# Performance work log

Hardware: AMD Instinct MI355X
Metric: run time of the kernel (lower is better)

Reference implementation:

```python
import jax, jax.numpy as jnp
import numpy as np

N, E, F, H = 50000, 800000, 128, 128

def silu(v):
    return v * jax.nn.sigmoid(v)

def setup_inputs() -> dict:
    key = jax.random.key(0)
    ks = jax.random.split(key, 16)
    def lin(k, fan_in, fan_out):
        s = 1.0 / np.sqrt(fan_in)
        kw, kb = jax.random.split(k)
        W = jax.random.uniform(kw, (fan_in, fan_out), jnp.float32, -s, s)
        b = jax.random.uniform(kb, (fan_out,), jnp.float32, -s, s)
        return W, b
    x = jax.random.normal(ks[0], (N, F), jnp.float32)
    pos = jax.random.normal(ks[1], (N, 3), jnp.float32)
    edge_index = jax.random.randint(ks[2], (2, E), 0, N, jnp.int64)
    We1, be1 = lin(ks[3], 2 * F + 1, H)
    We2, be2 = lin(ks[4], H, H)
    Wn1, bn1 = lin(ks[5], F + H, H)
    Wn2, bn2 = lin(ks[6], H, F)
    Wc, bc = lin(ks[7], H, 1)
    return {"x": x, "pos": pos, "We1": We1, "be1": be1, "We2": We2, "be2": be2,
            "Wn1": Wn1, "bn1": bn1, "Wn2": Wn2, "bn2": bn2, "Wc": Wc, "bc": bc,
            "edge_index": edge_index}

def reference(x, pos, We1, be1, We2, be2, Wn1, bn1, Wn2, bn2, Wc, bc, edge_index):
    row, col = edge_index[0], edge_index[1]
    rij = pos[row] - pos[col]                      # [E,3]
    dij = jnp.sum(rij ** 2, axis=-1, keepdims=True)  # [E,1]
    edge_input = jnp.concatenate([x[row], x[col], dij], axis=-1)  # [E,2F+1]
    m_ij = silu(silu(edge_input @ We1 + be1) @ We2 + be2)          # [E,H]
    agg = jax.ops.segment_sum(m_ij, row, num_segments=N)          # [N,H]
    x_new = silu(jnp.concatenate([x, agg], axis=-1) @ Wn1 + bn1) @ Wn2 + bn2  # [N,F]
    w_ij = silu(m_ij @ Wc + bc)                    # [E,1]
    trans = rij * w_ij                             # [E,3]
    delta = jax.ops.segment_sum(trans, row, num_segments=N)       # [N,3]
    pos_new = pos + 0.01 * delta
    return (x_new, pos_new)
```

## Files before the change

### kernel.cpp

```cpp
#include <hip/hip_runtime.h>
#include <hip/hip_bf16.h>
#include <stdint.h>
#include <string.h>

#define NN 50000
#define NE 800000
#define SCAN_B 200
#define SCAN_CH 250

typedef short bf8_t __attribute__((ext_vector_type(8)));
typedef float f32x4 __attribute__((ext_vector_type(4)));

__device__ __forceinline__ float silu_f(float v) {
    return v * __builtin_amdgcn_rcpf(1.0f + __expf(-v));
}

__device__ __forceinline__ unsigned int pack2bf(float a, float b) {
    __hip_bfloat162 h = __float22bfloat162_rn(make_float2(a, b));
    unsigned int u; memcpy(&u, &h, 4);
    return u;
}

__device__ __forceinline__ float bf_lo(unsigned int u) { return __uint_as_float(u << 16); }
__device__ __forceinline__ float bf_hi(unsigned int u) { return __uint_as_float(u & 0xffff0000u); }

union U4B { uint4 u; bf8_t b; };
__device__ __forceinline__ bf8_t as_bf8(uint4 u) { U4B x; x.u = u; return x.b; }

__global__ __launch_bounds__(64) void prep_w(const float* __restrict__ We1,
                                             const float* __restrict__ We2,
                                             const float* __restrict__ Wn1,
                                             const float* __restrict__ Wn2,
                                             unsigned short* __restrict__ wf1,
                                             unsigned short* __restrict__ wf2,
                                             unsigned short* __restrict__ wfn1,
                                             unsigned short* __restrict__ wfn2) {
    int b = blockIdx.x, lane = threadIdx.x;
    int q = lane >> 4, c = lane & 15;
    const float* W; unsigned short* dst; int f;
    if (b < 64)       { W = We1; f = b;       dst = wf1  + (size_t)f * 512; }
    else if (b < 96)  { W = We2; f = b - 64;  dst = wf2  + (size_t)f * 512; }
    else if (b < 160) { W = Wn1; f = b - 96;  dst = wfn1 + (size_t)f * 512; }
    else              { W = Wn2; f = b - 160; dst = wfn2 + (size_t)f * 512; }
    int s = f >> 3, mf = f & 7;
    int k0 = s * 32 + q * 8, col = mf * 16 + c;
    float v[8];
    #pragma unroll
    for (int i = 0; i < 8; ++i) v[i] = W[(size_t)(k0 + i) * 128 + col];
    uint4 o;
    o.x = pack2bf(v[0], v[1]); o.y = pack2bf(v[2], v[3]);
    o.z = pack2bf(v[4], v[5]); o.w = pack2bf(v[6], v[7]);
    *(uint4*)(dst + lane * 8) = o;
}

__global__ __launch_bounds__(256, 4) void prep_node(
    const float* __restrict__ x, const int* __restrict__ ei,
    const unsigned short* __restrict__ wf1, const float* __restrict__ be1,
    unsigned short* __restrict__ xbf, unsigned short* __restrict__ zbf,
    unsigned short* __restrict__ ybf, int* __restrict__ cnt)
{
    const int tid = threadIdx.x;
    const int n0 = blockIdx.x * 64;
    const char* w1 = (const char*)wf1;

    {
        int e0 = (blockIdx.x * 256 + tid) * 4;
        if (e0 < NE) {
            int4 r4 = *(const int4*)(ei + e0);
            atomicAdd(&cnt[r4.x], 1); atomicAdd(&cnt[r4.y], 1);
            atomicAdd(&cnt[r4.z], 1); atomicAdd(&cnt[r4.w], 1);
        }
    }

    {
        int node = n0 + (tid >> 2);
        if (node < NN) {
            const float* src = x + (size_t)node * 128 + (tid & 3) * 32;
            unsigned short* dst = xbf + (size_t)node * 128 + (tid & 3) * 32;
            #pragma unroll
            for (int j = 0; j < 4; ++j) {
                float4 v0 = *(const float4*)(src + j * 8);
                float4 v1 = *(const float4*)(src + j * 8 + 4);
                uint4 o;
                o.x = pack2bf(v0.x, v0.y); o.y = pack2bf(v0.z, v0.w);
                o.z = pack2bf(v1.x, v1.y); o.w = pack2bf(v1.z, v1.w);
                *(uint4*)(dst + j * 8) = o;
            }
        }
    }

    const int P = tid >> 6, lane = tid & 63;
    const int q = lane >> 4, e16 = lane & 15;
    const int oc_q = P * 32 + q * 4;

    int nloc[4]; unsigned nb[4];
    #pragma unroll
    for (int t = 0; t < 4; ++t) {
        int nl = t * 16 + e16; nloc[t] = nl;
        int node = n0 + nl; if (node >= NN) node = NN - 1;
        nb[t] = (unsigned)node;
    }

    f32x4 accz[2][4], accy[2][4];
    #pragma unroll
    for (int M = 0; M < 2; ++M) {
        float4 bi = *(const float4*)(be1 + oc_q + M * 16);
        #pragma unroll
        for (int t = 0; t < 4; ++t) {
            accz[M][t][0] = bi.x; accz[M][t][1] = bi.y; accz[M][t][2] = bi.z; accz[M][t][3] = bi.w;
            accy[M][t][0] = 0.f;  accy[M][t][1] = 0.f;  accy[M][t][2] = 0.f;  accy[M][t][3] = 0.f;
        }
    }

    #pragma unroll
    for (int s = 0; s < 4; ++s) {
        bf8_t bfr[4];
        #pragma unroll
        for (int t = 0; t < 4; ++t) {
            const float* src = x + ((size_t)nb[t]) * 128 + s * 32 + q * 8;
            float4 v0 = *(const float4*)src;
            float4 v1 = *(const float4*)(src + 4);
            uint4 o;
            o.x = pack2bf(v0.x, v0.y); o.y = pack2bf(v0.z, v0.w);
            o.z = pack2bf(v1.x, v1.y); o.w = pack2bf(v1.z, v1.w);
            bfr[t] = as_bf8(o);
        }
        #pragma unroll
        for (int M = 0; M < 2; ++M) {
            unsigned wz = ((unsigned)(s * 8 + P * 2 + M) << 10) + ((unsigned)lane << 4);
            unsigned wy = ((unsigned)((s + 4) * 8 + P * 2 + M) << 10) + ((unsigned)lane << 4);
            bf8_t afz = as_bf8(*(const uint4*)(w1 + wz));
            bf8_t afy = as_bf8(*(const uint4*)(w1 + wy));
            #pragma unroll
            for (int t = 0; t < 4; ++t) {
                accz[M][t] = __builtin_amdgcn_mfma_f32_16x16x32_bf16(afz, bfr[t], accz[M][t], 0, 0, 0);
                accy[M][t] = __builtin_amdgcn_mfma_f32_16x16x32_bf16(afy, bfr[t], accy[M][t], 0, 0, 0);
            }
        }
    }

    #pragma unroll
    for (int M = 0; M < 2; ++M) {
        #pragma unroll
        for (int t = 0; t < 4; ++t) {
            int node = n0 + nloc[t];
            if (node < NN) {
                uint2 pz, py;
                pz.x = pack2bf(accz[M][t][0], accz[M][t][1]);
                pz.y = pack2bf(accz[M][t][2], accz[M][t][3]);
                py.x = pack2bf(accy[M][t][0], accy[M][t][1]);
                py.y = pack2bf(accy[M][t][2], accy[M][t][3]);
                *(uint2*)(zbf + ((size_t)node << 7) + oc_q + M * 16) = pz;
                *(uint2*)(ybf + ((size_t)node << 7) + oc_q + M * 16) = py;
            }
        }
    }
}

__global__ __launch_bounds__(256) void scan_bsum(const int* __restrict__ cnt,
                                                 int* __restrict__ bsum) {
    __shared__ int red[4];
    int b = blockIdx.x, tid = threadIdx.x;
    int n = b * SCAN_CH + tid;
    int v = (tid < SCAN_CH) ? cnt[n] : 0;
    #pragma unroll
    for (int o = 32; o; o >>= 1) v += __shfl_down(v, o);
    if ((tid & 63) == 0) red[tid >> 6] = v;
    __syncthreads();
    if (tid == 0) bsum[b] = red[0] + red[1] + red[2] + red[3];
}

__global__ __launch_bounds__(256) void scan_write(const int* __restrict__ cnt,
                                                  const int* __restrict__ bsum,
                                                  int* __restrict__ off,
                                                  int* __restrict__ cur) {
    __shared__ int part[256];
    __shared__ int basered[4];
    int b = blockIdx.x, tid = threadIdx.x;
    int bv = (tid < b) ? bsum[tid] : 0;
    #pragma unroll
    for (int o = 32; o; o >>= 1) bv += __shfl_down(bv, o);
    if ((tid & 63) == 0) basered[tid >> 6] = bv;
    __syncthreads();
    int base = basered[0] + basered[1] + basered[2] + basered[3];
    int n = b * SCAN_CH + tid;
    int c = (tid < SCAN_CH) ? cnt[n] : 0;
    part[tid] = c;
    __syncthreads();
    #pragma unroll
    for (int d = 1; d < 256; d <<= 1) {
        int v = (tid >= d) ? part[tid - d] : 0;
        __syncthreads();
        part[tid] += v;
        __syncthreads();
    }
    if (tid < SCAN_CH) {
        int excl = base + part[tid] - c;
        off[n] = excl; cur[n] = excl;
    }
    if (b == SCAN_B - 1 && tid == SCAN_CH) off[NN] = NE;
}

__global__ __launch_bounds__(256) void egnn_scatter(const int* __restrict__ ei,
                                                    int* __restrict__ cur,
                                                    int2* __restrict__ rc_slot) {
    int e = blockIdx.x * 256 + threadIdx.x;
    if (e < NE) {
        int r = ei[e];
        int p = atomicAdd(&cur[r], 1);
        rc_slot[p] = make_int2(r, ei[NE + e]);
    }
}

__global__ __launch_bounds__(256, 4) void egnn_edge_mfma(
    const unsigned short* __restrict__ zbf, const unsigned short* __restrict__ ybf,
    const float* __restrict__ pos,
    const unsigned short* __restrict__ wf2,
    const float* __restrict__ We1,
    const float* __restrict__ be2, const float* __restrict__ Wc,
    const float* __restrict__ bc,
    const int2* __restrict__ rc_slot,
    float* __restrict__ agg, float* __restrict__ delta)
{
    __shared__ __align__(16) unsigned short HsBuf[9216];
    unsigned short* Hs = HsBuf;
    unsigned short* mT = HsBuf;
    __shared__ int   rows_s[64];
    __shared__ float rij_s[64][3];
    __shared__ float dij_s[64];
    __shared__ float wdot[64];
    __shared__ int   seg_node[64], seg_start[65];
    __shared__ unsigned long long smask;
    __shared__ int firstPartial, lastPartial;

    const int tid = threadIdx.x;
    const int e0 = blockIdx.x * 64;
    const char* zb = (const char*)zbf;
    const char* yb = (const char*)ybf;
    const char* w2 = (const char*)wf2;

    if (tid < 64) {
        int2 rc = rc_slot[e0 + tid];
        int r = rc.x;
        rows_s[tid] = r;
        float d = 0.f;
        #pragma unroll
        for (int k = 0; k < 3; ++k) {
            float rv = pos[r * 3 + k] - pos[rc.y * 3 + k];
            rij_s[tid][k] = rv; d += rv * rv;
        }
        dij_s[tid] = d;
        wdot[tid] = 0.f;
        seg_start[tid] = 64;
        if (tid == 0) seg_start[64] = 64;
        int prev = __shfl_up(r, 1);
        bool flag = (tid == 0) || (r != prev);
        unsigned long long b = __ballot(flag);
        int seg = __popcll(b & ((2ull << tid) - 1)) - 1;
        if (flag) { seg_node[seg] = r; seg_start[seg] = tid; }
        int r63 = __shfl(r, 63);
        if (tid == 0) {
            smask = b;
            firstPartial = (e0 > 0) && (rc_slot[e0 - 1].x == r);
            lastPartial  = (e0 + 64 < NE) && (rc_slot[e0 + 64].x == r63);
        }
    }

    const int P = tid >> 6, lane = tid & 63;
    const int q = lane >> 4, e16 = lane & 15;
    const int oc_q = P * 32 + q * 4;

    int eloc[4]; unsigned rb[4], cb[4];
    #pragma unroll
    for (int t = 0; t < 4; ++t) {
        int el = t * 16 + e16; eloc[t] = el;
        int2 rc = rc_slot[e0 + el];
        rb[t] = (unsigned)rc.x << 8;
        cb[t] = (unsigned)rc.y << 8;
    }

    uint2 uzr[2][4], uyr[2][4];
    #pragma unroll
    for (int M = 0; M < 2; ++M) {
        const unsigned cbyte = (unsigned)((oc_q + M * 16) << 1);
        #pragma unroll
        for (int t = 0; t < 4; ++t) {
            uzr[M][t] = *(const uint2*)(zb + rb[t] + cbyte);
            uyr[M][t] = *(const uint2*)(yb + cb[t] + cbyte);
        }
    }
    __syncthreads();

    #pragma unroll
    for (int M = 0; M < 2; ++M) {
        float4 w256 = *(const float4*)(We1 + (size_t)256 * 128 + oc_q + M * 16);
        #pragma unroll
        for (int t = 0; t < 4; ++t) {
            uint2 uz = uzr[M][t], uy = uyr[M][t];
            float d = dij_s[eloc[t]];
            float v0 = silu_f(bf_lo(uz.x) + bf_lo(uy.x) + d * w256.x);
            float v1 = silu_f(bf_hi(uz.x) + bf_hi(uy.x) + d * w256.y);
            float v2 = silu_f(bf_lo(uz.y) + bf_lo(uy.y) + d * w256.z);
            float v3 = silu_f(bf_hi(uz.y) + bf_hi(uy.y) + d * w256.w);
            uint2 pk; pk.x = pack2bf(v0, v1); pk.y = pack2bf(v2, v3);
            *(uint2*)(Hs + eloc[t] * 136 + oc_q + M * 16) = pk;
        }
    }
    __syncthreads();

    f32x4 acc2[2][4];
    #pragma unroll
    for (int M = 0; M < 2; ++M) {
        float4 bi = *(const float4*)(be2 + oc_q + M * 16);
        #pragma unroll
        for (int t = 0; t < 4; ++t) { acc2[M][t][0] = bi.x; acc2[M][t][1] = bi.y; acc2[M][t][2] = bi.z; acc2[M][t][3] = bi.w; }
    }

    #pragma unroll
    for (int s = 0; s < 4; ++s) {
        bf8_t bfr[4];
        #pragma unroll
        for (int t = 0; t < 4; ++t)
            bfr[t] = as_bf8(*(const uint4*)(Hs + eloc[t] * 136 + s * 32 + q * 8));
        __builtin_amdgcn_s_setprio(1);
        #pragma unroll
        for (int M = 0; M < 2; ++M) {
            unsigned woff = ((unsigned)(s * 8 + P * 2 + M) << 10) + ((unsigned)lane << 4);
            bf8_t af = as_bf8(*(const uint4*)(w2 + woff));
            #pragma unroll
            for (int t = 0; t < 4; ++t)
                acc2[M][t] = __builtin_amdgcn_mfma_f32_16x16x32_bf16(af, bfr[t], acc2[M][t], 0, 0, 0);
        }
        __builtin_amdgcn_s_setprio(0);
    }
    __syncthreads();

    {
        float4 wcA = *(const float4*)(Wc + oc_q);
        float4 wcB = *(const float4*)(Wc + oc_q + 16);
        float part[4];
        #pragma unroll
        for (int t = 0; t < 4; ++t) part[t] = 0.f;

        #pragma unroll
        for (int M = 0; M < 2; ++M) {
            float4 wc = (M == 0) ? wcA : wcB;
            int cbase = oc_q + M * 16;
            #pragma unroll
            for (int t = 0; t < 4; ++t) {
                float v0 = silu_f(acc2[M][t][0]);
                float v1 = silu_f(acc2[M][t][1]);
                float v2 = silu_f(acc2[M][t][2]);
                float v3 = silu_f(acc2[M][t][3]);
                part[t] += v0 * wc.x + v1 * wc.y + v2 * wc.z + v3 * wc.w;
                unsigned ua = pack2bf(v0, v1), ub = pack2bf(v2, v3);
                int slot = eloc[t];
                mT[(cbase + 0) * 72 + slot] = (unsigned short)ua;
                mT[(cbase + 1) * 72 + slot] = (unsigned short)(ua >> 16);
                mT[(cbase + 2) * 72 + slot] = (unsigned short)ub;
                mT[(cbase + 3) * 72 + slot] = (unsigned short)(ub >> 16);
            }
        }
        #pragma unroll
        for (int t = 0; t < 4; ++t) {
            float p = part[t];
            p += __shfl_xor(p, 16);
            p += __shfl_xor(p, 32);
            if (q == 0) atomicAdd(&wdot[eloc[t]], p);
        }
    }
    __syncthreads();

    {
        const int wv = tid >> 6, l = tid & 63;
        const int cA = l & 15, kq = l >> 4;
        const int nseg = __popcll(smask);

        if (nseg <= 16) {
            const int st = seg_start[cA];
            const int en = seg_start[cA + 1] == 64 && cA + 1 == nseg ? seg_start[cA + 1] : seg_start[cA + 1];
            f32x4 accd[2];
            #pragma unroll
            for (int c2 = 0; c2 < 2; ++c2) { accd[c2][0] = 0.f; accd[c2][1] = 0.f; accd[c2][2] = 0.f; accd[c2][3] = 0.f; }
            #pragma unroll
            for (int kt = 0; kt < 2; ++kt) {
                bf8_t aS;
                #pragma unroll
                for (int i = 0; i < 8; ++i) {
                    int k = kt * 32 + kq * 8 + i;
                    aS[i] = (k >= st && k < en) ? (short)0x3F80 : (short)0;
                }
                #pragma unroll
                for (int c2 = 0; c2 < 2; ++c2) {
                    int ct = wv * 2 + c2;
                    bf8_t bM = as_bf8(*(const uint4*)(mT + (ct * 16 + cA) * 72 + kt * 32 + kq * 8));
                    accd[c2] = __builtin_amdgcn_mfma_f32_16x16x32_bf16(aS, bM, accd[c2], 0, 0, 0);
                }
            }
            #pragma unroll
            for (int c2 = 0; c2 < 2; ++c2) {
                int ct = wv * 2 + c2;
                #pragma unroll
                for (int r = 0; r < 4; ++r) {
                    int sg = kq * 4 + r;
                    if (sg < nseg) {
                        float v = accd[c2][r];
                        int node = seg_node[sg];
                        bool partial = (sg == 0 && firstPartial) || (sg == nseg - 1 && lastPartial);
                        float* dst = agg + (size_t)node * 128 + ct * 16 + cA;
                        if (partial) atomicAdd(dst, v); else *dst = v;
                    }
                }
            }
        } else if (wv * 16 < nseg) {
            const int seg = wv * 16 + cA;
            const int st = seg_start[seg];
            const int en = seg_start[seg + 1];
            f32x4 accd[8];
            #pragma unroll
            for (int ct = 0; ct < 8; ++ct) { accd[ct][0] = 0.f; accd[ct][1] = 0.f; accd[ct][2] = 0.f; accd[ct][3] = 0.f; }
            #pragma unroll
            for (int kt = 0; kt < 2; ++kt) {
                bf8_t aS;
                #pragma unroll
                for (int i = 0; i < 8; ++i) {
                    int k = kt * 32 + kq * 8 + i;
                    aS[i] = (k >= st && k < en) ? (short)0x3F80 : (short)0;
                }
                #pragma unroll
                for (int ct = 0; ct < 8; ++ct) {
                    bf8_t bM = as_bf8(*(const uint4*)(mT + (ct * 16 + cA) * 72 + kt * 32 + kq * 8));
                    accd[ct] = __builtin_amdgcn_mfma_f32_16x16x32_bf16(aS, bM, accd[ct], 0, 0, 0);
                }
            }
            #pragma unroll
            for (int ct = 0; ct < 8; ++ct) {
                #pragma unroll
                for (int r = 0; r < 4; ++r) {
                    int sg = wv * 16 + kq * 4 + r;
                    if (sg < nseg) {
                        float v = accd[ct][r];
                        int node = seg_node[sg];
                        bool partial = (sg == 0 && firstPartial) || (sg == nseg - 1 && lastPartial);
                        float* dst = agg + (size_t)node * 128 + ct * 16 + cA;
                        if (partial) atomicAdd(dst, v); else *dst = v;
                    }
                }
            }
        }

        if (tid < nseg) {
            float bcv = bc[0];
            int start = seg_start[tid];
            int end = (tid + 1 < nseg) ? seg_start[tid + 1] : 64;
            float d0 = 0.f, d1 = 0.f, d2 = 0.f;
            for (int s2 = start; s2 < end; ++s2) {
                float wgt = silu_f(wdot[s2] + bcv);
                d0 += rij_s[s2][0] * wgt;
                d1 += rij_s[s2][1] * wgt;
                d2 += rij_s[s2][2] * wgt;
            }
            int node = seg_node[tid];
            bool partial = (tid == 0 && firstPartial) || (tid == nseg - 1 && lastPartial);
            float* dd = delta + (size_t)node * 3;
            if (partial) { atomicAdd(dd, d0); atomicAdd(dd + 1, d1); atomicAdd(dd + 2, d2); }
            else         { dd[0] = d0; dd[1] = d1; dd[2] = d2; }
        }
    }
}

__global__ __launch_bounds__(256, 4) void egnn_node_mfma(
    const unsigned short* __restrict__ xbf, const float* __restrict__ agg,
    const float* __restrict__ delta, const float* __restrict__ pos,
    const unsigned short* __restrict__ wfn1, const unsigned short* __restrict__ wfn2,
    const float* __restrict__ bn1, const float* __restrict__ bn2,
    float* __restrict__ out)
{
    __shared__ unsigned short Hs[64 * 136];

    const int tid = threadIdx.x;
    const int n0 = blockIdx.x * 64;
    const char* xb = (const char*)xbf;
    const char* ab = (const char*)agg;
    const char* w1 = (const char*)wfn1;
    const char* w2 = (const char*)wfn2;

    if (tid < 192) {
        int n = n0 + tid / 3, d = tid - 3 * (tid / 3);
        if (n < NN)
            out[(size_t)NN * 128 + (size_t)n * 3 + d] =
                pos[(size_t)n * 3 + d] + 0.01f * delta[(size_t)n * 3 + d];
    }

    const int P = tid >> 6, lane = tid & 63;
    const int q = lane >> 4, e16 = lane & 15;
    const int oc_q = P * 32 + q * 4;

    int nloc[4]; unsigned nb[4];
    #pragma unroll
    for (int t = 0; t < 4; ++t) {
        int nl = t * 16 + e16; nloc[t] = nl;
        int node = n0 + nl; if (node >= NN) node = NN - 1;
        nb[t] = (unsigned)node;
    }

    f32x4 acc[2][4];
    #pragma unroll
    for (int M = 0; M < 2; ++M) {
        float4 bi = *(const float4*)(bn1 + oc_q + M * 16);
        #pragma unroll
        for (int t = 0; t < 4; ++t) { acc[M][t][0] = bi.x; acc[M][t][1] = bi.y; acc[M][t][2] = bi.z; acc[M][t][3] = bi.w; }
    }

    #pragma unroll
    for (int s = 0; s < 8; ++s) {
        bf8_t bfr[4];
        #pragma unroll
        for (int t = 0; t < 4; ++t) {
            if (s < 4) {
                unsigned noff = (nb[t] << 8) + (unsigned)((s & 3) * 64 + q * 16);
                bfr[t] = as_bf8(*(const uint4*)(xb + noff));
            } else {
                unsigned aoff = (nb[t] << 9) + (unsigned)(((s & 3) * 32 + q * 8) * 4);
                float4 a0 = *(const float4*)(ab + aoff);
                float4 a1 = *(const float4*)(ab + aoff + 16);
                uint4 o;
                o.x = pack2bf(a0.x, a0.y); o.y = pack2bf(a0.z, a0.w);
                o.z = pack2bf(a1.x, a1.y); o.w = pack2bf(a1.z, a1.w);
                bfr[t] = as_bf8(o);
            }
        }
        #pragma unroll
        for (int M = 0; M < 2; ++M) {
            unsigned woff = ((unsigned)(s * 8 + P * 2 + M) << 10) + ((unsigned)lane << 4);
            bf8_t af = as_bf8(*(const uint4*)(w1 + woff));
            #pragma unroll
            for (int t = 0; t < 4; ++t)
                acc[M][t] = __builtin_amdgcn_mfma_f32_16x16x32_bf16(af, bfr[t], acc[M][t], 0, 0, 0);
        }
    }

    #pragma unroll
    for (int M = 0; M < 2; ++M) {
        #pragma unroll
        for (int t = 0; t < 4; ++t) {
            float v0 = silu_f(acc[M][t][0]);
            float v1 = silu_f(acc[M][t][1]);
            float v2 = silu_f(acc[M][t][2]);
            float v3 = silu_f(acc[M][t][3]);
            uint2 pk; pk.x = pack2bf(v0, v1); pk.y = pack2bf(v2, v3);
            *(uint2*)(Hs + nloc[t] * 136 + oc_q + M * 16) = pk;
        }
    }
    __syncthreads();

    f32x4 acc2[2][4];
    #pragma unroll
    for (int M = 0; M < 2; ++M) {
        float4 bi = *(const float4*)(bn2 + oc_q + M * 16);
        #pragma unroll
        for (int t = 0; t < 4; ++t) { acc2[M][t][0] = bi.x; acc2[M][t][1] = bi.y; acc2[M][t][2] = bi.z; acc2[M][t][3] = bi.w; }
    }

    #pragma unroll
    for (int s = 0; s < 4; ++s) {
        bf8_t bfr[4];
        #pragma unroll
        for (int t = 0; t < 4; ++t)
            bfr[t] = as_bf8(*(const uint4*)(Hs + nloc[t] * 136 + s * 32 + q * 8));
        #pragma unroll
        for (int M = 0; M < 2; ++M) {
            unsigned woff = ((unsigned)(s * 8 + P * 2 + M) << 10) + ((unsigned)lane << 4);
            bf8_t af = as_bf8(*(const uint4*)(w2 + woff));
            #pragma unroll
            for (int t = 0; t < 4; ++t)
                acc2[M][t] = __builtin_amdgcn_mfma_f32_16x16x32_bf16(af, bfr[t], acc2[M][t], 0, 0, 0);
        }
    }

    #pragma unroll
    for (int M = 0; M < 2; ++M) {
        #pragma unroll
        for (int t = 0; t < 4; ++t) {
            int node = n0 + nloc[t];
            if (node < NN) {
                float4 v; v.x = acc2[M][t][0]; v.y = acc2[M][t][1]; v.z = acc2[M][t][2]; v.w = acc2[M][t][3];
                *(float4*)(out + (size_t)node * 128 + oc_q + M * 16) = v;
            }
        }
    }
}

extern "C" void kernel_launch(void* const* d_in, const int* in_sizes, int n_in,
                              void* d_out, int out_size, void* d_ws, size_t ws_size,
                              hipStream_t stream)
{
    const float* x   = (const float*)d_in[0];
    const float* pos = (const float*)d_in[1];
    const float* We1 = (const float*)d_in[2];
    const float* be1 = (const float*)d_in[3];
    const float* We2 = (const float*)d_in[4];
    const float* be2 = (const float*)d_in[5];
    const float* Wn1 = (const float*)d_in[6];
    const float* bn1 = (const float*)d_in[7];
    const float* Wn2 = (const float*)d_in[8];
    const float* bn2 = (const float*)d_in[9];
    const float* Wc  = (const float*)d_in[10];
    const float* bc  = (const float*)d_in[11];
    const int*   ei  = (const int*)d_in[12];
    float* out = (float*)d_out;

    char* p = (char*)d_ws;
    float* agg   = (float*)p;                  p += (size_t)NN * 128 * 4;
    float* delta = (float*)p;                  p += (size_t)NN * 3 * 4;
    int* cnt     = (int*)p;                    p += (size_t)NN * 4;
    unsigned short* xbf = (unsigned short*)p;  p += (size_t)NN * 128 * 2;
    unsigned short* zbf = (unsigned short*)p;  p += (size_t)NN * 128 * 2;
    unsigned short* ybf = (unsigned short*)p;  p += (size_t)NN * 128 * 2;
    unsigned short* wf1  = (unsigned short*)p; p += 65536;
    unsigned short* wf2  = (unsigned short*)p; p += 32768;
    unsigned short* wfn1 = (unsigned short*)p; p += 65536;
    unsigned short* wfn2 = (unsigned short*)p; p += 32768;
    int* off   = (int*)p;                      p += (size_t)(NN + 1) * 4 + 12;
    int* cur   = (int*)p;                      p += (size_t)NN * 4;
    int* bsum  = (int*)p;                      p += (size_t)SCAN_B * 4;
    int2* rc_slot = (int2*)p;

    hipMemsetAsync(agg, 0, ((size_t)NN * 128 + (size_t)NN * 3 + NN) * 4, stream);

    prep_w<<<192, 64, 0, stream>>>(We1, We2, Wn1, Wn2, wf1, wf2, wfn1, wfn2);
    prep_node<<<(NN + 63) / 64, 256, 0, stream>>>(x, ei, wf1, be1, xbf, zbf, ybf, cnt);
    scan_bsum<<<SCAN_B, 256, 0, stream>>>(cnt, bsum);
    scan_write<<<SCAN_B, 256, 0, stream>>>(cnt, bsum, off, cur);
    egnn_scatter<<<NE / 256, 256, 0, stream>>>(ei, cur, rc_slot);
    egnn_edge_mfma<<<NE / 64, 256, 0, stream>>>(zbf, ybf, pos, wf2, We1, be2,
                                                Wc, bc, rc_slot, agg, delta);
    egnn_node_mfma<<<(NN + 63) / 64, 256, 0, stream>>>(xbf, agg, delta, pos,
                                                       wfn1, wfn2, bn1, bn2, out);
}
```

Measured before the change: 298.4 us.

## Precompute node x@Wn1 in prep kernel, remap edge blocks per XCD, vectorise scatter

The x-half of the node MLP's first layer (x@Wn1[:F]+bn1) now runs in the prep kernel as a third GEMM pass and is stored in bf16. The node kernel then seeds its accumulators from it and only does the agg half, which drops the xbf buffer and halves the node GEMM K. The edge kernel remaps block IDs so each XCD gets a contiguous chunk of edges, for better L2 locality on sorted segments, and its occupancy hint is raised from 4 to 5. The CSR scatter now handles four edges per thread with int4 loads. The trade-offs are extra bf16 rounding of the partial sum and lower occupancy in prep_node.

```diff
diff --git a/kernel.cpp b/kernel.cpp
--- a/kernel.cpp
+++ b/kernel.cpp
@@ -53,65 +53,18 @@
     *(uint4*)(dst + lane * 8) = o;
 }
 
-__global__ __launch_bounds__(256, 4) void prep_node(
-    const float* __restrict__ x, const int* __restrict__ ei,
-    const unsigned short* __restrict__ wf1, const float* __restrict__ be1,
-    unsigned short* __restrict__ xbf, unsigned short* __restrict__ zbf,
-    unsigned short* __restrict__ ybf, int* __restrict__ cnt)
+__device__ __forceinline__ void node_gemm_pass(
+    const float* __restrict__ x, const unsigned* nb, const int* nloc, int n0,
+    const char* __restrict__ wbase, const float* __restrict__ bias,
+    unsigned short* __restrict__ dst, int P, int lane, int q, int oc_q)
 {
-    const int tid = threadIdx.x;
-    const int n0 = blockIdx.x * 64;
-    const char* w1 = (const char*)wf1;
-
-    {
-        int e0 = (blockIdx.x * 256 + tid) * 4;
-        if (e0 < NE) {
-            int4 r4 = *(const int4*)(ei + e0);
-            atomicAdd(&cnt[r4.x], 1); atomicAdd(&cnt[r4.y], 1);
-            atomicAdd(&cnt[r4.z], 1); atomicAdd(&cnt[r4.w], 1);
-        }
-    }
-
-    {
-        int node = n0 + (tid >> 2);
-        if (node < NN) {
-            const float* src = x + (size_t)node * 128 + (tid & 3) * 32;
-            unsigned short* dst = xbf + (size_t)node * 128 + (tid & 3) * 32;
-            #pragma unroll
-            for (int j = 0; j < 4; ++j) {
-                float4 v0 = *(const float4*)(src + j * 8);
-                float4 v1 = *(const float4*)(src + j * 8 + 4);
-                uint4 o;
-                o.x = pack2bf(v0.x, v0.y); o.y = pack2bf(v0.z, v0.w);
-                o.z = pack2bf(v1.x, v1.y); o.w = pack2bf(v1.z, v1.w);
-                *(uint4*)(dst + j * 8) = o;
-            }
-        }
-    }
-
-    const int P = tid >> 6, lane = tid & 63;
-    const int q = lane >> 4, e16 = lane & 15;
-    const int oc_q = P * 32 + q * 4;
-
-    int nloc[4]; unsigned nb[4];
-    #pragma unroll
-    for (int t = 0; t < 4; ++t) {
-        int nl = t * 16 + e16; nloc[t] = nl;
-        int node = n0 + nl; if (node >= NN) node = NN - 1;
-        nb[t] = (unsigned)node;
-    }
-
-    f32x4 accz[2][4], accy[2][4];
-    #pragma unroll
-    for (int M = 0; M < 2; ++M) {
-        float4 bi = *(const float4*)(be1 + oc_q + M * 16);
-        #pragma unroll
-        for (int t = 0; t < 4; ++t) {
-            accz[M][t][0] = bi.x; accz[M][t][1] = bi.y; accz[M][t][2] = bi.z; accz[M][t][3] = bi.w;
-            accy[M][t][0] = 0.f;  accy[M][t][1] = 0.f;  accy[M][t][2] = 0.f;  accy[M][t][3] = 0.f;
-        }
-    }
-
+    f32x4 acc[2][4];
+    #pragma unroll
+    for (int M = 0; M < 2; ++M) {
+        float4 bi = bias ? *(const float4*)(bias + oc_q + M * 16) : make_float4(0.f, 0.f, 0.f, 0.f);
+        #pragma unroll
+        for (int t = 0; t < 4; ++t) { acc[M][t][0] = bi.x; acc[M][t][1] = bi.y; acc[M][t][2] = bi.z; acc[M][t][3] = bi.w; }
+    }
     #pragma unroll
     for (int s = 0; s < 4; ++s) {
         bf8_t bfr[4];
@@ -127,34 +80,62 @@
         }
         #pragma unroll
         for (int M = 0; M < 2; ++M) {
-            unsigned wz = ((unsigned)(s * 8 + P * 2 + M) << 10) + ((unsigned)lane << 4);
-            unsigned wy = ((unsigned)((s + 4) * 8 + P * 2 + M) << 10) + ((unsigned)lane << 4);
-            bf8_t afz = as_bf8(*(const uint4*)(w1 + wz));
-            bf8_t afy = as_bf8(*(const uint4*)(w1 + wy));
-            #pragma unroll
-            for (int t = 0; t < 4; ++t) {
-                accz[M][t] = __builtin_amdgcn_mfma_f32_16x16x32_bf16(afz, bfr[t], accz[M][t], 0, 0, 0);
-                accy[M][t] = __builtin_amdgcn_mfma_f32_16x16x32_bf16(afy, bfr[t], accy[M][t], 0, 0, 0);
-            }
-        }
-    }
-
+            unsigned woff = ((unsigned)(s * 8 + P * 2 + M) << 10) + ((unsigned)lane << 4);
+            bf8_t af = as_bf8(*(const uint4*)(wbase + woff));
+            #pragma unroll
+            for (int t = 0; t < 4; ++t)
+                acc[M][t] = __builtin_amdgcn_mfma_f32_16x16x32_bf16(af, bfr[t], acc[M][t], 0, 0, 0);
+        }
+    }
     #pragma unroll
     for (int M = 0; M < 2; ++M) {
         #pragma unroll
         for (int t = 0; t < 4; ++t) {
             int node = n0 + nloc[t];
             if (node < NN) {
-                uint2 pz, py;
-                pz.x = pack2bf(accz[M][t][0], accz[M][t][1]);
-                pz.y = pack2bf(accz[M][t][2], accz[M][t][3]);
-                py.x = pack2bf(accy[M][t][0], accy[M][t][1]);
-                py.y = pack2bf(accy[M][t][2], accy[M][t][3]);
-                *(uint2*)(zbf + ((size_t)node << 7) + oc_q + M * 16) = pz;
-                *(uint2*)(ybf + ((size_t)node << 7) + oc_q + M * 16) = py;
-            }
-        }
-    }
+                uint2 pz;
+                pz.x = pack2bf(acc[M][t][0], acc[M][t][1]);
+                pz.y = pack2bf(acc[M][t][2], acc[M][t][3]);
+                *(uint2*)(dst + ((size_t)node << 7) + oc_q + M * 16) = pz;
+            }
+        }
+    }
+}
+
+__global__ __launch_bounds__(256, 2) void prep_node(
+    const float* __restrict__ x, const int* __restrict__ ei,
+    const unsigned short* __restrict__ wf1, const unsigned short* __restrict__ wfn1,
+    const float* __restrict__ be1, const float* __restrict__ bn1,
+    unsigned short* __restrict__ zbf, unsigned short* __restrict__ ybf,
+    unsigned short* __restrict__ znbf, int* __restrict__ cnt)
+{
+    const int tid = threadIdx.x;
+    const int n0 = blockIdx.x * 64;
+
+    {
+        int e0 = (blockIdx.x * 256 + tid) * 4;
+        if (e0 < NE) {
+            int4 r4 = *(const int4*)(ei + e0);
+            atomicAdd(&cnt[r4.x], 1); atomicAdd(&cnt[r4.y], 1);
+            atomicAdd(&cnt[r4.z], 1); atomicAdd(&cnt[r4.w], 1);
+        }
+    }
+
+    const int P = tid >> 6, lane = tid & 63;
+    const int q = lane >> 4, e16 = lane & 15;
+    const int oc_q = P * 32 + q * 4;
+
+    int nloc[4]; unsigned nb[4];
+    #pragma unroll
+    for (int t = 0; t < 4; ++t) {
+        int nl = t * 16 + e16; nloc[t] = nl;
+        int node = n0 + nl; if (node >= NN) node = NN - 1;
+        nb[t] = (unsigned)node;
+    }
+
+    node_gemm_pass(x, nb, nloc, n0, (const char*)wf1,           be1, zbf,  P, lane, q, oc_q);
+    node_gemm_pass(x, nb, nloc, n0, (const char*)wf1 + (32u << 10), nullptr, ybf, P, lane, q, oc_q);
+    node_gemm_pass(x, nb, nloc, n0, (const char*)wfn1,          bn1, znbf, P, lane, q, oc_q);
 }
 
 __global__ __launch_bounds__(256) void scan_bsum(const int* __restrict__ cnt,
@@ -204,15 +185,18 @@
 __global__ __launch_bounds__(256) void egnn_scatter(const int* __restrict__ ei,
                                                     int* __restrict__ cur,
                                                     int2* __restrict__ rc_slot) {
-    int e = blockIdx.x * 256 + threadIdx.x;
+    int e = (blockIdx.x * 256 + threadIdx.x) * 4;
     if (e < NE) {
-        int r = ei[e];
-        int p = atomicAdd(&cur[r], 1);
-        rc_slot[p] = make_int2(r, ei[NE + e]);
-    }
-}
-
-__global__ __launch_bounds__(256, 4) void egnn_edge_mfma(
+        int4 r4 = *(const int4*)(ei + e);
+        int4 c4 = *(const int4*)(ei + NE + e);
+        int p0 = atomicAdd(&cur[r4.x], 1); rc_slot[p0] = make_int2(r4.x, c4.x);
+        int p1 = atomicAdd(&cur[r4.y], 1); rc_slot[p1] = make_int2(r4.y, c4.y);
+        int p2 = atomicAdd(&cur[r4.z], 1); rc_slot[p2] = make_int2(r4.z, c4.z);
+        int p3 = atomicAdd(&cur[r4.w], 1); rc_slot[p3] = make_int2(r4.w, c4.w);
+    }
+}
+
+__global__ __launch_bounds__(256, 5) void egnn_edge_mfma(
     const unsigned short* __restrict__ zbf, const unsigned short* __restrict__ ybf,
     const float* __restrict__ pos,
     const unsigned short* __restrict__ wf2,
@@ -234,7 +218,10 @@
     __shared__ int firstPartial, lastPartial;
 
     const int tid = threadIdx.x;
-    const int e0 = blockIdx.x * 64;
+    const int bid = blockIdx.x;
+    const int xcd = bid & 7, ii = bid >> 3;
+    const int blk = (xcd < 4 ? xcd * 1563 : 4 * 1563 + (xcd - 4) * 1562) + ii;
+    const int e0 = blk * 64;
     const char* zb = (const char*)zbf;
     const char* yb = (const char*)ybf;
     const char* w2 = (const char*)wf2;
@@ -378,7 +365,7 @@
 
         if (nseg <= 16) {
             const int st = seg_start[cA];
-            const int en = seg_start[cA + 1] == 64 && cA + 1 == nseg ? seg_start[cA + 1] : seg_start[cA + 1];
+            const int en = seg_start[cA + 1];
             f32x4 accd[2];
             #pragma unroll
             for (int c2 = 0; c2 < 2; ++c2) { accd[c2][0] = 0.f; accd[c2][1] = 0.f; accd[c2][2] = 0.f; accd[c2][3] = 0.f; }
@@ -470,17 +457,17 @@
 }
 
 __global__ __launch_bounds__(256, 4) void egnn_node_mfma(
-    const unsigned short* __restrict__ xbf, const float* __restrict__ agg,
+    const unsigned short* __restrict__ znbf, const float* __restrict__ agg,
     const float* __restrict__ delta, const float* __restrict__ pos,
     const unsigned short* __restrict__ wfn1, const unsigned short* __restrict__ wfn2,
-    const float* __restrict__ bn1, const float* __restrict__ bn2,
+    const float* __restrict__ bn2,
     float* __restrict__ out)
 {
     __shared__ unsigned short Hs[64 * 136];
 
     const int tid = threadIdx.x;
     const int n0 = blockIdx.x * 64;
-    const char* xb = (const char*)xbf;
+    const char* zn = (const char*)znbf;
     const char* ab = (const char*)agg;
     const char* w1 = (const char*)wfn1;
     const char* w2 = (const char*)wfn2;
@@ -507,32 +494,31 @@
     f32x4 acc[2][4];
     #pragma unroll
     for (int M = 0; M < 2; ++M) {
-        float4 bi = *(const float4*)(bn1 + oc_q + M * 16);
-        #pragma unroll
-        for (int t = 0; t < 4; ++t) { acc[M][t][0] = bi.x; acc[M][t][1] = bi.y; acc[M][t][2] = bi.z; acc[M][t][3] = bi.w; }
-    }
-
-    #pragma unroll
-    for (int s = 0; s < 8; ++s) {
+        const unsigned cbyte = (unsigned)((oc_q + M * 16) << 1);
+        #pragma unroll
+        for (int t = 0; t < 4; ++t) {
+            uint2 uz = *(const uint2*)(zn + (nb[t] << 8) + cbyte);
+            acc[M][t][0] = bf_lo(uz.x); acc[M][t][1] = bf_hi(uz.x);
+            acc[M][t][2] = bf_lo(uz.y); acc[M][t][3] = bf_hi(uz.y);
+        }
+    }
+
+    #pragma unroll
+    for (int s = 0; s < 4; ++s) {
         bf8_t bfr[4];
         #pragma unroll
         for (int t = 0; t < 4; ++t) {
-            if (s < 4) {
-                unsigned noff = (nb[t] << 8) + (unsigned)((s & 3) * 64 + q * 16);
-                bfr[t] = as_bf8(*(const uint4*)(xb + noff));
-            } else {
-                unsigned aoff = (nb[t] << 9) + (unsigned)(((s & 3) * 32 + q * 8) * 4);
-                float4 a0 = *(const float4*)(ab + aoff);
-                float4 a1 = *(const float4*)(ab + aoff + 16);
-                uint4 o;
-                o.x = pack2bf(a0.x, a0.y); o.y = pack2bf(a0.z, a0.w);
-                o.z = pack2bf(a1.x, a1.y); o.w = pack2bf(a1.z, a1.w);
-                bfr[t] = as_bf8(o);
-            }
+            unsigned aoff = (nb[t] << 9) + (unsigned)((s * 32 + q * 8) * 4);
+            float4 a0 = *(const float4*)(ab + aoff);
+            float4 a1 = *(const float4*)(ab + aoff + 16);
+            uint4 o;
+            o.x = pack2bf(a0.x, a0.y); o.y = pack2bf(a0.z, a0.w);
+            o.z = pack2bf(a1.x, a1.y); o.w = pack2bf(a1.z, a1.w);
+            bfr[t] = as_bf8(o);
         }
         #pragma unroll
         for (int M = 0; M < 2; ++M) {
-            unsigned woff = ((unsigned)(s * 8 + P * 2 + M) << 10) + ((unsigned)lane << 4);
+            unsigned woff = ((unsigned)((s + 4) * 8 + P * 2 + M) << 10) + ((unsigned)lane << 4);
             bf8_t af = as_bf8(*(const uint4*)(w1 + woff));
             #pragma unroll
             for (int t = 0; t < 4; ++t)
@@ -614,7 +600,7 @@
     float* agg   = (float*)p;                  p += (size_t)NN * 128 * 4;
     float* delta = (float*)p;                  p += (size_t)NN * 3 * 4;
     int* cnt     = (int*)p;                    p += (size_t)NN * 4;
-    unsigned short* xbf = (unsigned short*)p;  p += (size_t)NN * 128 * 2;
+    unsigned short* znbf = (unsigned short*)p; p += (size_t)NN * 128 * 2;
     unsigned short* zbf = (unsigned short*)p;  p += (size_t)NN * 128 * 2;
     unsigned short* ybf = (unsigned short*)p;  p += (size_t)NN * 128 * 2;
     unsigned short* wf1  = (unsigned short*)p; p += 65536;
@@ -629,12 +615,13 @@
     hipMemsetAsync(agg, 0, ((size_t)NN * 128 + (size_t)NN * 3 + NN) * 4, stream);
 
     prep_w<<<192, 64, 0, stream>>>(We1, We2, Wn1, Wn2, wf1, wf2, wfn1, wfn2);
-    prep_node<<<(NN + 63) / 64, 256, 0, stream>>>(x, ei, wf1, be1, xbf, zbf, ybf, cnt);
+    prep_node<<<(NN + 63) / 64, 256, 0, stream>>>(x, ei, wf1, wfn1, be1, bn1,
+                                                  zbf, ybf, znbf, cnt);
     scan_bsum<<<SCAN_B, 256, 0, stream>>>(cnt, bsum);
     scan_write<<<SCAN_B, 256, 0, stream>>>(cnt, bsum, off, cur);
-    egnn_scatter<<<NE / 256, 256, 0, stream>>>(ei, cur, rc_slot);
+    egnn_scatter<<<(NE / 4 + 255) / 256, 256, 0, stream>>>(ei, cur, rc_slot);
     egnn_edge_mfma<<<NE / 64, 256, 0, stream>>>(zbf, ybf, pos, wf2, We1, be2,
                                                 Wc, bc, rc_slot, agg, delta);
-    egnn_node_mfma<<<(NN + 63) / 64, 256, 0, stream>>>(xbf, agg, delta, pos,
-                                                       wfn1, wfn2, bn1, bn2, out);
-}
+    egnn_node_mfma<<<(NN + 63) / 64, 256, 0, stream>>>(znbf, agg, delta, pos,
+                                                       wfn1, wfn2, bn2, out);
+}
```

New measurement: 294.5 us. No clear change (-1.3%).
